# Optimization experiments

Measured on AMD Instinct MI355X. Metric: run time of the kernel, lower is better.

The kernel has to match this reference:

```python
import jax, jax.numpy as jnp
import numpy as np

ALPHA = 3.0
EPS = 1e-30


def setup_inputs() -> dict:
    key = jax.random.key(0)
    ks = jax.random.split(key, 12)
    B, N, T, D = 16, 2048, 96, 32
    s = 1.0 / np.sqrt(D)
    inp = {
        "spatial_nodes": jax.random.normal(ks[0], (B, N, D), dtype=jnp.float32),
        "temporal_nodes": jax.random.normal(ks[1], (B, T, D), dtype=jnp.float32),
        # ss graph linears (no bias)
        "W_ss1": jax.random.normal(ks[2], (D, D), dtype=jnp.float32) * s,
        "W_ss2": jax.random.normal(ks[3], (D, D), dtype=jnp.float32) * s,
        # 'st' attention (query/key linears with bias); value linear is unused in forward
        "Wq_st": jax.random.normal(ks[4], (D, D), dtype=jnp.float32) * s,
        "bq_st": jax.random.normal(ks[5], (D,), dtype=jnp.float32) * s,
        "Wk_st": jax.random.normal(ks[6], (D, D), dtype=jnp.float32) * s,
        "bk_st": jax.random.normal(ks[7], (D,), dtype=jnp.float32) * s,
        # 'ts' attention
        "Wq_ts": jax.random.normal(ks[8], (D, D), dtype=jnp.float32) * s,
        "bq_ts": jax.random.normal(ks[9], (D,), dtype=jnp.float32) * s,
        "Wk_ts": jax.random.normal(ks[10], (D, D), dtype=jnp.float32) * s,
        "bk_ts": jax.random.normal(ks[11], (D,), dtype=jnp.float32) * s,
    }
    return inp


def _uni_adj(a):
    # relu -> global-max normalize -> tanh -> nan_to_num (matches GraphConstructor.uni_adj)
    r = jax.nn.relu(a)
    div = jnp.max(r)  # global max across the whole tensor (incl. batch), as in torch
    out = jnp.tanh(jnp.where(div > 0, r / (div + EPS), r))
    return jnp.nan_to_num(out)


def reference(spatial_nodes, temporal_nodes, W_ss1, W_ss2,
              Wq_st, bq_st, Wk_st, bk_st, Wq_ts, bq_ts, Wk_ts, bk_ts):
    # forward() detaches both inputs
    s = jax.lax.stop_gradient(spatial_nodes)  # (B, N, D)
    t = jax.lax.stop_gradient(temporal_nodes)  # (B, T, D)
    N = s.shape[1]

    emb = jnp.concatenate([s, t], axis=1)  # (B, N+T, D)
    adj = jnp.einsum('bnf,bmf->bnm', emb, emb)  # (B, N+T, N+T)

    def ss_graph(x1, x2):
        n1 = jnp.tanh(ALPHA * (x1 @ W_ss1.T))
        n2 = jnp.tanh(ALPHA * (x2 @ W_ss2.T))
        return ALPHA * (jnp.einsum('bnf,bmf->bnm', n1, n2)
                        - jnp.einsum('bnf,bmf->bnm', n2, n1))

    def attn_graph(x1, x2, Wq, bq, Wk, bk):
        q = x1 @ Wq.T + bq
        k = x2 @ Wk.T + bk
        return jnp.einsum('bnf,bmf->bnm', q, k)

    ss_adj = adj[:, :N, :N] + ss_graph(s, s)
    st_adj = adj[:, :N, N:] + attn_graph(s, t, Wq_st, bq_st, Wk_st, bk_st)
    ts_adj = adj[:, N:, :N] + attn_graph(t, s, Wq_ts, bq_ts, Wk_ts, bk_ts)
    tt_adj = adj[:, N:, N:]

    ss_u = _uni_adj(ss_adj)
    st_u = _uni_adj(st_adj)
    ts_u = _uni_adj(ts_adj)
    tt_u = jnp.triu(_uni_adj(tt_adj))  # tt_mask=True: upper-triangular (incl diag)

    top = jnp.concatenate([ss_u, st_u], axis=2)
    bot = jnp.concatenate([ts_u, tt_u], axis=2)
    return jnp.concatenate([top, bot], axis=1)  # (B, N+T, N+T)
```

## Files before the change

### kernel.cpp

```cpp
#include <hip/hip_runtime.h>
#include <math.h>

#define BATCH 16
#define NS 2048
#define NT 96
#define DIM 32
#define ROWL 2144
#define EPSV 1e-30f

#define FS_STRIDE 224
#define FT_STRIDE 96

typedef __attribute__((ext_vector_type(8))) short bf16x8;
typedef __attribute__((ext_vector_type(4))) float f32x4;

__device__ __forceinline__ ushort f2bf_rn(float x){
  uint u = __float_as_uint(x);
  return (ushort)((u + 0x7FFFu + ((u >> 16) & 1u)) >> 16);
}
__device__ __forceinline__ float bf2f(ushort h){
  return __uint_as_float(((uint)h) << 16);
}

__global__ __launch_bounds__(256) void feat_kernel(
    const float* __restrict__ sp, const float* __restrict__ tp,
    const float* __restrict__ Wss1, const float* __restrict__ Wss2,
    const float* __restrict__ Wqst, const float* __restrict__ bqst,
    const float* __restrict__ Wkst, const float* __restrict__ bkst,
    const float* __restrict__ Wqts, const float* __restrict__ bqts,
    const float* __restrict__ Wkts, const float* __restrict__ bkts,
    ushort* __restrict__ FShi, ushort* __restrict__ FSlo,
    ushort* __restrict__ FThi, ushort* __restrict__ FTlo)
{
  __shared__ float Wl[6*1056];
  __shared__ float bl[128];
  __shared__ float xl[8][32];
  const int tid = threadIdx.x;
  {
    const float* Ws[6] = {Wss1, Wss2, Wqst, Wkst, Wqts, Wkts};
    #pragma unroll
    for (int m = 0; m < 6; m++){
      const float* W = Ws[m];
      #pragma unroll
      for (int c = 0; c < 4; c++){
        int idx = c*256 + tid;
        Wl[m*1056 + (idx>>5)*33 + (idx&31)] = W[idx];
      }
    }
    if (tid < 32)        bl[tid] = bqst[tid];
    else if (tid < 64)   bl[tid] = bkst[tid-32];
    else if (tid < 96)   bl[tid] = bqts[tid-64];
    else if (tid < 128)  bl[tid] = bkts[tid-96];
  }
  const int rs = tid >> 5;
  const int f  = tid & 31;
  const int row = blockIdx.x*8 + rs;
  const int NROWS = BATCH*NS;
  const int TOT   = NROWS + BATCH*NT;
  const bool valid = row < TOT;
  const bool isS   = row < NROWS;
  if (valid){
    const float* xp = isS ? (sp + (size_t)row*DIM) : (tp + (size_t)(row-NROWS)*DIM);
    xl[rs][f] = xp[f];
  }
  __syncthreads();
  if (!valid) return;

  if (isS){
    float a1=0.f, a2=0.f, aq=0.f, ak=0.f;
    #pragma unroll
    for (int d=0; d<32; d++){
      float xv = xl[rs][d];
      a1 = fmaf(xv, Wl[0*1056 + f*33 + d], a1);
      a2 = fmaf(xv, Wl[1*1056 + f*33 + d], a2);
      aq = fmaf(xv, Wl[2*1056 + f*33 + d], aq);
      ak = fmaf(xv, Wl[5*1056 + f*33 + d], ak);
    }
    float n1 = tanhf(3.0f*a1);
    float n2 = tanhf(3.0f*a2);
    float vals[7];
    vals[0] = xl[rs][f];
    vals[1] = 3.0f*n1;
    vals[2] = -3.0f*n2;
    vals[3] = n2;
    vals[4] = n1;
    vals[5] = aq + bl[0  + f];
    vals[6] = ak + bl[96 + f];
    ushort* oh = FShi + (size_t)row*FS_STRIDE + f;
    ushort* ol = FSlo + (size_t)row*FS_STRIDE + f;
    #pragma unroll
    for (int sgm = 0; sgm < 7; sgm++){
      float x = vals[sgm];
      ushort h = f2bf_rn(x);
      oh[sgm*32] = h;
      ol[sgm*32] = f2bf_rn(x - bf2f(h));
    }
  } else {
    const int rt = row - NROWS;
    float aq=0.f, ak=0.f;
    #pragma unroll
    for (int d=0; d<32; d++){
      float xv = xl[rs][d];
      aq = fmaf(xv, Wl[4*1056 + f*33 + d], aq);
      ak = fmaf(xv, Wl[3*1056 + f*33 + d], ak);
    }
    float vals[3];
    vals[0] = xl[rs][f];
    vals[1] = aq + bl[64 + f];
    vals[2] = ak + bl[32 + f];
    ushort* oh = FThi + (size_t)rt*FT_STRIDE + f;
    ushort* ol = FTlo + (size_t)rt*FT_STRIDE + f;
    #pragma unroll
    for (int sgm = 0; sgm < 3; sgm++){
      float x = vals[sgm];
      ushort h = f2bf_rn(x);
      oh[sgm*32] = h;
      ol[sgm*32] = f2bf_rn(x - bf2f(h));
    }
  }
}

template<int NKB>
__global__ __launch_bounds__(256, 2) void adj_mfma(
    const ushort* __restrict__ Uhi, const ushort* __restrict__ Ulo, int ustride,
    int NI, int uo0, int uo1, int uo2,
    const ushort* __restrict__ Vhi, const ushort* __restrict__ Vlo, int vstride,
    int NJ, int vo0, int vo1, int vo2,
    float* __restrict__ out, int i0g, int j0g, float* __restrict__ maxslot)
{
  constexpr int ACELLS = 4*NKB*64;
  constexpr int BCELLS = 8*NKB*64;
  __shared__ __align__(16) ushort sAh[ACELLS*8];
  __shared__ __align__(16) ushort sAl[ACELLS*8];
  __shared__ __align__(16) ushort sBh[BCELLS*8];
  __shared__ __align__(16) ushort sBl[BCELLS*8];
  __shared__ float red[4];
  const int tid = threadIdx.x;
  const int b   = blockIdx.z;
  const int i0t = blockIdx.y*64;
  const int j0t = blockIdx.x*128;

  const ushort* Ubh = Uhi + (size_t)b*NI*ustride;
  const ushort* Ubl = Ulo + (size_t)b*NI*ustride;
  const ushort* Vbh = Vhi + (size_t)b*NJ*vstride;
  const ushort* Vbl = Vlo + (size_t)b*NJ*vstride;

  for (int u = tid; u < ACELLS; u += 256){
    int q   = u & 3;
    int t   = u >> 2;
    int r15 = t & 15;
    int t2  = t >> 4;
    int kb  = t2 % NKB;
    int g   = t2 / NKB;
    int so  = (kb == 0) ? uo0 : ((kb == 1) ? uo1 : uo2);
    int gr  = i0t + g*16 + r15;
    uint4 vh = make_uint4(0u,0u,0u,0u), vl = vh;
    if (gr < NI){
      const size_t base = (size_t)gr*ustride + so + q*8;
      vh = *(const uint4*)(Ubh + base);
      vl = *(const uint4*)(Ubl + base);
    }
    int dcell = (t2*4 + q)*16 + r15;
    *(uint4*)&sAh[dcell*8] = vh;
    *(uint4*)&sAl[dcell*8] = vl;
  }
  for (int u = tid; u < BCELLS; u += 256){
    int q   = u & 3;
    int t   = u >> 2;
    int r15 = t & 15;
    int t2  = t >> 4;
    int kb  = t2 % NKB;
    int g   = t2 / NKB;
    int so  = (kb == 0) ? vo0 : ((kb == 1) ? vo1 : vo2);
    int gr  = j0t + g*16 + r15;
    uint4 vh = make_uint4(0u,0u,0u,0u), vl = vh;
    if (gr < NJ){
      const size_t base = (size_t)gr*vstride + so + q*8;
      vh = *(const uint4*)(Vbh + base);
      vl = *(const uint4*)(Vbl + base);
    }
    int dcell = (t2*4 + q)*16 + r15;
    *(uint4*)&sBh[dcell*8] = vh;
    *(uint4*)&sBl[dcell*8] = vl;
  }
  __syncthreads();

  const int lane = tid & 63;
  const int w    = tid >> 6;
  const int wm   = w & 1;
  const int wn   = w >> 1;
  const int l15  = lane & 15;
  const int l4   = lane >> 4;

  f32x4 acc[2][4] = {};

  #pragma unroll
  for (int kb = 0; kb < NKB; ++kb){
    bf16x8 ah[2], al[2], bh[4], bl[4];
    #pragma unroll
    for (int m = 0; m < 2; m++){
      int off = ((2*wm + m)*NKB + kb)*512 + lane*8;
      ah[m] = *(const bf16x8*)&sAh[off];
      al[m] = *(const bf16x8*)&sAl[off];
    }
    #pragma unroll
    for (int n = 0; n < 4; n++){
      int off = ((4*wn + n)*NKB + kb)*512 + lane*8;
      bh[n] = *(const bf16x8*)&sBh[off];
      bl[n] = *(const bf16x8*)&sBl[off];
    }
    #pragma unroll
    for (int m = 0; m < 2; m++){
      #pragma unroll
      for (int n = 0; n < 4; n++){
        acc[m][n] = __builtin_amdgcn_mfma_f32_16x16x32_bf16(ah[m], bh[n], acc[m][n], 0,0,0);
        acc[m][n] = __builtin_amdgcn_mfma_f32_16x16x32_bf16(ah[m], bl[n], acc[m][n], 0,0,0);
        acc[m][n] = __builtin_amdgcn_mfma_f32_16x16x32_bf16(al[m], bh[n], acc[m][n], 0,0,0);
      }
    }
  }

  float lmax = 0.f;
  const size_t obase = (size_t)b*ROWL*ROWL;
  #pragma unroll
  for (int m = 0; m < 2; m++){
    int gi_base = i0t + wm*32 + m*16 + l4*4;
    #pragma unroll
    for (int r = 0; r < 4; r++){
      int gi = gi_base + r;
      if (gi < NI){
        const size_t rowb = obase + (size_t)(i0g+gi)*ROWL + j0g;
        #pragma unroll
        for (int n = 0; n < 4; n++){
          int gj = j0t + wn*64 + n*16 + l15;
          if (gj < NJ){
            float v = acc[m][n][r];
            out[rowb + gj] = v;
            lmax = fmaxf(lmax, v);
          }
        }
      }
    }
  }
  #pragma unroll
  for (int off = 32; off > 0; off >>= 1)
    lmax = fmaxf(lmax, __shfl_xor(lmax, off));
  if ((tid & 63) == 0) red[tid >> 6] = lmax;
  __syncthreads();
  if (tid == 0){
    float m4 = fmaxf(fmaxf(red[0], red[1]), fmaxf(red[2], red[3]));
    atomicMax((int*)maxslot, __float_as_int(m4));
  }
}

__device__ __forceinline__ float tanh01(float x){
  float e = __expf(2.0f*x);
  return __fdividef(e - 1.0f, e + 1.0f);
}
__device__ __forceinline__ float4 uni4(float4 v, float r){
  v.x = tanh01(fmaxf(v.x,0.f)*r);
  v.y = tanh01(fmaxf(v.y,0.f)*r);
  v.z = tanh01(fmaxf(v.z,0.f)*r);
  v.w = tanh01(fmaxf(v.w,0.f)*r);
  return v;
}

__global__ __launch_bounds__(256) void uni_kernel(float* __restrict__ out,
                                                  const float* __restrict__ mx)
{
  const int row = blockIdx.x;
  const int i   = row % ROWL;
  const bool top = (i < NS);
  const float rl = 1.0f/((top ? mx[0] : mx[2]) + EPSV);
  const float rr = 1.0f/((top ? mx[1] : mx[3]) + EPSV);
  float4* rowp = (float4*)(out + (size_t)row*ROWL);
  const int tid = threadIdx.x;

  rowp[tid]       = uni4(rowp[tid],       rl);
  rowp[tid + 256] = uni4(rowp[tid + 256], rl);

  if (tid < 24){
    float4 v = uni4(rowp[tid + 512], rr);
    if (!top){
      int il = i - NS;
      int jl = 4*tid;
      if (jl+0 < il) v.x = 0.f;
      if (jl+1 < il) v.y = 0.f;
      if (jl+2 < il) v.z = 0.f;
      if (jl+3 < il) v.w = 0.f;
    }
    rowp[tid + 512] = v;
  }
}

extern "C" void kernel_launch(void* const* d_in, const int* in_sizes, int n_in,
                              void* d_out, int out_size, void* d_ws, size_t ws_size,
                              hipStream_t stream)
{
  const float* sp   = (const float*)d_in[0];
  const float* tp   = (const float*)d_in[1];
  const float* Wss1 = (const float*)d_in[2];
  const float* Wss2 = (const float*)d_in[3];
  const float* Wqst = (const float*)d_in[4];
  const float* bqst = (const float*)d_in[5];
  const float* Wkst = (const float*)d_in[6];
  const float* bkst = (const float*)d_in[7];
  const float* Wqts = (const float*)d_in[8];
  const float* bqts = (const float*)d_in[9];
  const float* Wkts = (const float*)d_in[10];
  const float* bkts = (const float*)d_in[11];
  float* out  = (float*)d_out;
  float* wsf  = (float*)d_ws;
  float* maxs = wsf;

  const size_t SHROWS = (size_t)BATCH*NS;
  const size_t STROWS = (size_t)BATCH*NT;
  ushort* FShi = (ushort*)(wsf + 16);
  ushort* FSlo = FShi + SHROWS*FS_STRIDE;
  ushort* FThi = FSlo + SHROWS*FS_STRIDE;
  ushort* FTlo = FThi + STROWS*FT_STRIDE;

  feat_kernel<<<dim3((BATCH*(NS+NT))/8), 256, 0, stream>>>(
      sp,tp,Wss1,Wss2,Wqst,bqst,Wkst,bkst,Wqts,bqts,Wkts,bkts,
      FShi,FSlo,FThi,FTlo);

  adj_mfma<3><<<dim3(16,32,BATCH), 256, 0, stream>>>(
      FShi,FSlo,FS_STRIDE,NS, 0,32,64,
      FShi,FSlo,FS_STRIDE,NS, 0,96,128,
      out, 0,0, maxs+0);

  adj_mfma<2><<<dim3(1,32,BATCH), 256, 0, stream>>>(
      FShi,FSlo,FS_STRIDE,NS, 0,160,0,
      FThi,FTlo,FT_STRIDE,NT, 0,64,0,
      out, 0,NS, maxs+1);

  adj_mfma<2><<<dim3(16,2,BATCH), 256, 0, stream>>>(
      FThi,FTlo,FT_STRIDE,NT, 0,32,0,
      FShi,FSlo,FS_STRIDE,NS, 0,192,0,
      out, NS,0, maxs+2);

  adj_mfma<1><<<dim3(1,2,BATCH), 256, 0, stream>>>(
      FThi,FTlo,FT_STRIDE,NT, 0,0,0,
      FThi,FTlo,FT_STRIDE,NT, 0,0,0,
      out, NS,NS, maxs+3);

  uni_kernel<<<BATCH*ROWL, 256, 0, stream>>>(out, maxs);
}
```

Measured before the change: 548.7 us.

## Recompute adjacency GEMM in second pass with fused normalize-tanh epilogue

Splits the adjacency computation into a max-only pass and a recompute pass that applies relu, global-max normalization, tanh and the upper-triangular mask directly in the MFMA epilogue. This removes the separate elementwise kernel and the write-read-rewrite round trip of the large output tensor. The cost is running the small-K GEMMs twice.

```diff
diff --git a/kernel.cpp b/kernel.cpp
--- a/kernel.cpp
+++ b/kernel.cpp
@@ -120,13 +120,19 @@
   }
 }
 
-template<int NKB>
+__device__ __forceinline__ float tanh01(float x){
+  float e = __expf(2.0f*x);
+  return __fdividef(e - 1.0f, e + 1.0f);
+}
+
+template<int NKB, int MODE>
 __global__ __launch_bounds__(256, 2) void adj_mfma(
     const ushort* __restrict__ Uhi, const ushort* __restrict__ Ulo, int ustride,
     int NI, int uo0, int uo1, int uo2,
     const ushort* __restrict__ Vhi, const ushort* __restrict__ Vlo, int vstride,
     int NJ, int vo0, int vo1, int vo2,
-    float* __restrict__ out, int i0g, int j0g, float* __restrict__ maxslot)
+    float* __restrict__ out, int i0g, int j0g, float* __restrict__ maxslot,
+    int triu)
 {
   constexpr int ACELLS = 4*NKB*64;
   constexpr int BCELLS = 8*NKB*64;
@@ -220,76 +226,47 @@
     }
   }
 
-  float lmax = 0.f;
-  const size_t obase = (size_t)b*ROWL*ROWL;
-  #pragma unroll
-  for (int m = 0; m < 2; m++){
-    int gi_base = i0t + wm*32 + m*16 + l4*4;
-    #pragma unroll
-    for (int r = 0; r < 4; r++){
-      int gi = gi_base + r;
-      if (gi < NI){
-        const size_t rowb = obase + (size_t)(i0g+gi)*ROWL + j0g;
+  if (MODE == 0){
+    float lmax = 0.f;
+    #pragma unroll
+    for (int m = 0; m < 2; m++)
+      #pragma unroll
+      for (int n = 0; n < 4; n++)
         #pragma unroll
-        for (int n = 0; n < 4; n++){
-          int gj = j0t + wn*64 + n*16 + l15;
-          if (gj < NJ){
-            float v = acc[m][n][r];
-            out[rowb + gj] = v;
-            lmax = fmaxf(lmax, v);
+        for (int r = 0; r < 4; r++)
+          lmax = fmaxf(lmax, acc[m][n][r]);
+    #pragma unroll
+    for (int off = 32; off > 0; off >>= 1)
+      lmax = fmaxf(lmax, __shfl_xor(lmax, off));
+    if ((tid & 63) == 0) red[tid >> 6] = lmax;
+    __syncthreads();
+    if (tid == 0){
+      float m4 = fmaxf(fmaxf(red[0], red[1]), fmaxf(red[2], red[3]));
+      atomicMax((int*)maxslot, __float_as_int(m4));
+    }
+  } else {
+    const float rinv = 1.0f/(maxslot[0] + EPSV);
+    const size_t obase = (size_t)b*ROWL*ROWL;
+    #pragma unroll
+    for (int m = 0; m < 2; m++){
+      int gi_base = i0t + wm*32 + m*16 + l4*4;
+      #pragma unroll
+      for (int r = 0; r < 4; r++){
+        int gi = gi_base + r;
+        if (gi < NI){
+          const size_t rowb = obase + (size_t)(i0g+gi)*ROWL + j0g;
+          #pragma unroll
+          for (int n = 0; n < 4; n++){
+            int gj = j0t + wn*64 + n*16 + l15;
+            if (gj < NJ){
+              float v = tanh01(fmaxf(acc[m][n][r], 0.f)*rinv);
+              if (triu && gj < gi) v = 0.f;
+              out[rowb + gj] = v;
+            }
           }
         }
       }
     }
-  }
-  #pragma unroll
-  for (int off = 32; off > 0; off >>= 1)
-    lmax = fmaxf(lmax, __shfl_xor(lmax, off));
-  if ((tid & 63) == 0) red[tid >> 6] = lmax;
-  __syncthreads();
-  if (tid == 0){
-    float m4 = fmaxf(fmaxf(red[0], red[1]), fmaxf(red[2], red[3]));
-    atomicMax((int*)maxslot, __float_as_int(m4));
-  }
-}
-
-__device__ __forceinline__ float tanh01(float x){
-  float e = __expf(2.0f*x);
-  return __fdividef(e - 1.0f, e + 1.0f);
-}
-__device__ __forceinline__ float4 uni4(float4 v, float r){
-  v.x = tanh01(fmaxf(v.x,0.f)*r);
-  v.y = tanh01(fmaxf(v.y,0.f)*r);
-  v.z = tanh01(fmaxf(v.z,0.f)*r);
-  v.w = tanh01(fmaxf(v.w,0.f)*r);
-  return v;
-}
-
-__global__ __launch_bounds__(256) void uni_kernel(float* __restrict__ out,
-                                                  const float* __restrict__ mx)
-{
-  const int row = blockIdx.x;
-  const int i   = row % ROWL;
-  const bool top = (i < NS);
-  const float rl = 1.0f/((top ? mx[0] : mx[2]) + EPSV);
-  const float rr = 1.0f/((top ? mx[1] : mx[3]) + EPSV);
-  float4* rowp = (float4*)(out + (size_t)row*ROWL);
-  const int tid = threadIdx.x;
-
-  rowp[tid]       = uni4(rowp[tid],       rl);
-  rowp[tid + 256] = uni4(rowp[tid + 256], rl);
-
-  if (tid < 24){
-    float4 v = uni4(rowp[tid + 512], rr);
-    if (!top){
-      int il = i - NS;
-      int jl = 4*tid;
-      if (jl+0 < il) v.x = 0.f;
-      if (jl+1 < il) v.y = 0.f;
-      if (jl+2 < il) v.z = 0.f;
-      if (jl+3 < il) v.w = 0.f;
-    }
-    rowp[tid + 512] = v;
   }
 }
 
@@ -324,25 +301,37 @@
       sp,tp,Wss1,Wss2,Wqst,bqst,Wkst,bkst,Wqts,bqts,Wkts,bkts,
       FShi,FSlo,FThi,FTlo);
 
-  adj_mfma<3><<<dim3(16,32,BATCH), 256, 0, stream>>>(
+  adj_mfma<3,0><<<dim3(16,32,BATCH), 256, 0, stream>>>(
       FShi,FSlo,FS_STRIDE,NS, 0,32,64,
       FShi,FSlo,FS_STRIDE,NS, 0,96,128,
-      out, 0,0, maxs+0);
-
-  adj_mfma<2><<<dim3(1,32,BATCH), 256, 0, stream>>>(
+      out, 0,0, maxs+0, 0);
+  adj_mfma<2,0><<<dim3(1,32,BATCH), 256, 0, stream>>>(
       FShi,FSlo,FS_STRIDE,NS, 0,160,0,
       FThi,FTlo,FT_STRIDE,NT, 0,64,0,
-      out, 0,NS, maxs+1);
-
-  adj_mfma<2><<<dim3(16,2,BATCH), 256, 0, stream>>>(
+      out, 0,NS, maxs+1, 0);
+  adj_mfma<2,0><<<dim3(16,2,BATCH), 256, 0, stream>>>(
       FThi,FTlo,FT_STRIDE,NT, 0,32,0,
       FShi,FSlo,FS_STRIDE,NS, 0,192,0,
-      out, NS,0, maxs+2);
-
-  adj_mfma<1><<<dim3(1,2,BATCH), 256, 0, stream>>>(
+      out, NS,0, maxs+2, 0);
+  adj_mfma<1,0><<<dim3(1,2,BATCH), 256, 0, stream>>>(
       FThi,FTlo,FT_STRIDE,NT, 0,0,0,
       FThi,FTlo,FT_STRIDE,NT, 0,0,0,
-      out, NS,NS, maxs+3);
-
-  uni_kernel<<<BATCH*ROWL, 256, 0, stream>>>(out, maxs);
-}
+      out, NS,NS, maxs+3, 0);
+
+  adj_mfma<3,1><<<dim3(16,32,BATCH), 256, 0, stream>>>(
+      FShi,FSlo,FS_STRIDE,NS, 0,32,64,
+      FShi,FSlo,FS_STRIDE,NS, 0,96,128,
+      out, 0,0, maxs+0, 0);
+  adj_mfma<2,1><<<dim3(1,32,BATCH), 256, 0, stream>>>(
+      FShi,FSlo,FS_STRIDE,NS, 0,160,0,
+      FThi,FTlo,FT_STRIDE,NT, 0,64,0,
+      out, 0,NS, maxs+1, 0);
+  adj_mfma<2,1><<<dim3(16,2,BATCH), 256, 0, stream>>>(
+      FThi,FTlo,FT_STRIDE,NT, 0,32,0,
+      FShi,FSlo,FS_STRIDE,NS, 0,192,0,
+      out, NS,0, maxs+2, 0);
+  adj_mfma<1,1><<<dim3(1,2,BATCH), 256, 0, stream>>>(
+      FThi,FTlo,FT_STRIDE,NT, 0,0,0,
+      FThi,FTlo,FT_STRIDE,NT, 0,0,0,
+      out, NS,NS, maxs+3, 1);
+}
```

New measurement: 578.4 us. 1.05x slower.
